# Optimization experiments

Measured on AMD Instinct MI355X. Metric: run time of the kernel, lower is better.

## Reference

```python
import jax, jax.numpy as jnp
import numpy as np

N = 100000        # nodes
E_RAND = 1600000  # random edges (avg degree 16)
D_IN = 64
D_OUT = 64


def setup_inputs() -> dict:
    key = jax.random.key(0)
    k1, k2, k3, k4, k5 = jax.random.split(key, 5)
    x = jax.random.normal(k1, (N, D_IN), dtype=jnp.float32)
    rows = jax.random.randint(k2, (E_RAND,), 0, N)
    cols = jax.random.randint(k3, (E_RAND,), 0, N)
    loops = jnp.arange(N)  # self loops appended at the end (matches remove+add_self_loops order)
    edge_index = jnp.stack([jnp.concatenate([rows, loops]),
                            jnp.concatenate([cols, loops])]).astype(jnp.int64)
    W = (jax.random.normal(k4, (D_IN, D_OUT), dtype=jnp.float32) / np.float32(np.sqrt(D_IN)))
    b = jax.random.normal(k5, (D_OUT,), dtype=jnp.float32) * 0.01
    return {"x": x, "edge_index": edge_index, "W": W, "b": b}


def reference(x, edge_index, W, b):
    row, col = edge_index[0], edge_index[1]
    # lin(x[row]) == (x @ W + b)[row]; transform once then gather (cheaper, same math)
    xl = x @ W + b                      # [N, D_OUT]
    x_i = xl[row]                       # [E, D_OUT] gather by destination
    x_j = xl[col]                       # [E, D_OUT] gather by source
    alpha = jnp.sum(x_i * x_j, axis=-1)  # [E] per-edge score
    alpha = jax.nn.leaky_relu(alpha, negative_slope=0.2)
    # segment-wise softmax over neighborhoods keyed by row
    m = jax.ops.segment_max(alpha, row, num_segments=N)
    m = jnp.where(jnp.isfinite(m), m, 0.0)   # isolated nodes -> -inf max, neutralize
    e = jnp.exp(alpha - m[row])
    s = jax.ops.segment_sum(e, row, num_segments=N)
    alpha = e / (s[row] + 1e-16)
    # dropout(p=0.6) skipped: reference runs in eval mode (deterministic)
    out = jax.ops.segment_sum(x_j * alpha[:, None], row, num_segments=N)  # [N, D_OUT]
    return out
```

## Files before the change

### kernel.cpp

```cpp
#include <hip/hip_runtime.h>
#include <hip/hip_bf16.h>


#define LEAKY_SLOPE 0.2f
#define BK_SHIFT 5
#define BK_NODES 32
#define CAPB 960
#define CH 8192
#define NBP 3136
#define MAXK 8

typedef __attribute__((ext_vector_type(8))) short short8;
typedef __attribute__((ext_vector_type(4))) float f32x4;

struct HiLo { short hi, lo; };

__device__ __forceinline__ HiLo split2(float f) {
    HiLo r;
    unsigned u = __float_as_uint(f);
    r.hi = (short)(u >> 16);
    float fh = __uint_as_float(u & 0xFFFF0000u);
    r.lo = (short)(__float_as_uint(f - fh) >> 16);
    return r;
}

__global__ __launch_bounds__(1024) void k_hist(const int* __restrict__ row,
                                               unsigned short* __restrict__ cntg,
                                               int E, int NB) {
    __shared__ int hc[NBP];
    int tid = threadIdx.x;
    for (int i = tid; i < NBP; i += 1024) hc[i] = 0;
    __syncthreads();
    int e0 = (int)blockIdx.x * CH;
    int e1 = min(E, e0 + CH);
    for (int e = e0 + tid; e < e1; e += 1024)
        atomicAdd(&hc[row[e] >> BK_SHIFT], 1);
    __syncthreads();
    unsigned short* orow = cntg + (size_t)blockIdx.x * NBP;
    for (int i = tid; i < NB; i += 1024) orow[i] = (unsigned short)hc[i];
}

__global__ __launch_bounds__(256) void k_tot(unsigned short* __restrict__ cntg,
                                             int* __restrict__ tot,
                                             int NB, int nch) {
    int wavegid = (((int)blockIdx.x * 256) + (int)threadIdx.x) >> 6;
    int lane = threadIdx.x & 63;
    int b = wavegid;
    if (b >= NB) return;

    int K = (nch + 63) >> 6;
    int v[MAXK];
    int s = 0;
    int c0 = lane * K;
#pragma unroll
    for (int k = 0; k < MAXK; ++k) {
        if (k < K) {
            int c = c0 + k;
            v[k] = (c < nch) ? (int)cntg[(size_t)c * NBP + b] : 0;
        }
    }
#pragma unroll
    for (int k = 0; k < MAXK; ++k) {
        if (k < K) { int t = v[k]; v[k] = s; s += t; }
    }
    int inc = s;
#pragma unroll
    for (int o = 1; o < 64; o <<= 1) {
        int t = __shfl_up(inc, o, 64);
        if (lane >= o) inc += t;
    }
    int exc = inc - s;
#pragma unroll
    for (int k = 0; k < MAXK; ++k) {
        if (k < K) {
            int c = c0 + k;
            if (c < nch)
                cntg[(size_t)c * NBP + b] = (unsigned short)(v[k] + exc);
        }
    }
    if (lane == 63) tot[b] = inc;
}

__global__ __launch_bounds__(1024) void k_base(const int* __restrict__ tot,
                                               int* __restrict__ base,
                                               int NB, int E) {
    __shared__ int segsum[16];
    int tid = threadIdx.x, lane = tid & 63, wid = tid >> 6;
    int segbeg = tid * 4;
    int loc[4];
    int s = 0;
#pragma unroll
    for (int k = 0; k < 4; ++k) {
        int i = segbeg + k;
        int t = (i < NB) ? tot[i] : 0;
        loc[k] = s; s += t;
    }
    int v = s;
#pragma unroll
    for (int o = 1; o < 64; o <<= 1) {
        int t = __shfl_up(v, o, 64);
        if (lane >= o) v += t;
    }
    if (lane == 63) segsum[wid] = v;
    __syncthreads();
    int woff = 0;
#pragma unroll
    for (int w = 0; w < 16; ++w) woff += (w < wid) ? segsum[w] : 0;
    int segoff = (v - s) + woff;
#pragma unroll
    for (int k = 0; k < 4; ++k) {
        int i = segbeg + k;
        if (i < NB) base[i] = loc[k] + segoff;
    }
    if (tid == 0) base[NB] = E;
}

union SLShMem {
    struct { short wt_hi[64 * 72]; short wt_lo[64 * 72]; } lin;
    struct { int pfx[NBP], pos[NBP]; } sc;
};

__global__ __launch_bounds__(1024) void k_scatlin(const float* __restrict__ x,
                                                  const float* __restrict__ W,
                                                  const float* __restrict__ b,
                                                  const int* __restrict__ row,
                                                  const int* __restrict__ col,
                                                  float* __restrict__ xl,
                                                  unsigned short* __restrict__ xlh,
                                                  const unsigned short* __restrict__ cntg,
                                                  const int* __restrict__ base,
                                                  unsigned* __restrict__ slab,
                                                  int N, int E, int NB,
                                                  int ntiles, int nsc, int nch) {
    __shared__ SLShMem sh;
    int tid = threadIdx.x;

    if ((int)blockIdx.x < nsc) {
        int cb = (int)blockIdx.x;
        int chunk = (nch % 8 == 0) ? (cb % 8) * (nch / 8) + cb / 8 : cb;

        const unsigned short* crow = cntg + (size_t)chunk * NBP;
        for (int i = tid; i < NB; i += 1024) {
            sh.sc.pfx[i] = base[i] + (int)crow[i];
            sh.sc.pos[i] = 0;
        }
        __syncthreads();

        int e0 = chunk * CH;
        int e1 = min(E, e0 + CH);
        for (int e = e0 + tid; e < e1; e += 1024) {
            int r = row[e], c = col[e];
            int bkt = r >> BK_SHIFT;
            int rank = atomicAdd(&sh.sc.pos[bkt], 1);
            slab[sh.sc.pfx[bkt] + rank] =
                ((unsigned)(r & (BK_NODES - 1)) << 17) | (unsigned)c;
        }
    } else {
        for (int i = tid; i < 4096; i += 1024) {
            int k = i >> 6, n = i & 63;
            HiLo h = split2(W[i]);
            sh.lin.wt_hi[n * 72 + k] = h.hi;
            sh.lin.wt_lo[n * 72 + k] = h.lo;
        }
        __syncthreads();

        int wave = tid >> 6, lane = tid & 63;
        int tile = ((int)blockIdx.x - nsc) * 16 + wave;
        if (tile >= ntiles) return;
        int node0 = tile * 16;
        int m = lane & 15;
        int quad = lane >> 4;

        f32x4 acc[4] = {{0.f, 0.f, 0.f, 0.f}, {0.f, 0.f, 0.f, 0.f},
                        {0.f, 0.f, 0.f, 0.f}, {0.f, 0.f, 0.f, 0.f}};

#pragma unroll
        for (int ks = 0; ks < 64; ks += 32) {
            const float* xr = x + (size_t)(node0 + m) * 64 + ks + quad * 8;
            float4 xa = *(const float4*)xr;
            float4 xb = *(const float4*)(xr + 4);
            short8 a_hi, a_lo;
            {
                HiLo h0 = split2(xa.x), h1 = split2(xa.y), h2 = split2(xa.z), h3 = split2(xa.w);
                HiLo h4 = split2(xb.x), h5 = split2(xb.y), h6 = split2(xb.z), h7 = split2(xb.w);
                a_hi[0] = h0.hi; a_lo[0] = h0.lo;  a_hi[1] = h1.hi; a_lo[1] = h1.lo;
                a_hi[2] = h2.hi; a_lo[2] = h2.lo;  a_hi[3] = h3.hi; a_lo[3] = h3.lo;
                a_hi[4] = h4.hi; a_lo[4] = h4.lo;  a_hi[5] = h5.hi; a_lo[5] = h5.lo;
                a_hi[6] = h6.hi; a_lo[6] = h6.lo;  a_hi[7] = h7.hi; a_lo[7] = h7.lo;
            }
#pragma unroll
            for (int g = 0; g < 4; ++g) {
                int n = g * 16 + m;
                int off = n * 72 + ks + quad * 8;
                short8 bh = *(const short8*)&sh.lin.wt_hi[off];
                short8 bl = *(const short8*)&sh.lin.wt_lo[off];
                acc[g] = __builtin_amdgcn_mfma_f32_16x16x32_bf16(a_hi, bh, acc[g], 0, 0, 0);
                acc[g] = __builtin_amdgcn_mfma_f32_16x16x32_bf16(a_lo, bh, acc[g], 0, 0, 0);
                acc[g] = __builtin_amdgcn_mfma_f32_16x16x32_bf16(a_hi, bl, acc[g], 0, 0, 0);
            }
        }

#pragma unroll
        for (int g = 0; g < 4; ++g) {
            float bias = b[g * 16 + m];
#pragma unroll
            for (int r = 0; r < 4; ++r) {
                int node = node0 + quad * 4 + r;
                if (node < N) {
                    float v = acc[g][r] + bias;
                    xl[(size_t)node * 64 + g * 16 + m] = v;
                    xlh[(size_t)node * 64 + g * 16 + m] =
                        (unsigned short)(__float_as_uint(v) >> 16);
                }
            }
        }
    }
}

template <int CTRL>
__device__ __forceinline__ float dpp_add(float x) {
    int y = __builtin_amdgcn_update_dpp(0, __float_as_int(x), CTRL, 0xF, 0xF, true);
    return x + __int_as_float(y);
}

__device__ __forceinline__ float red8(float d) {
    d = dpp_add<0xB1>(d);
    d = dpp_add<0x4E>(d);
    d = dpp_add<0x141>(d);
    return d;
}

__device__ __forceinline__ void bf8_to_f8(uint4 u, float4& a, float4& b) {
    a.x = __uint_as_float(u.x << 16);
    a.y = __uint_as_float(u.x & 0xFFFF0000u);
    a.z = __uint_as_float(u.y << 16);
    a.w = __uint_as_float(u.y & 0xFFFF0000u);
    b.x = __uint_as_float(u.z << 16);
    b.y = __uint_as_float(u.z & 0xFFFF0000u);
    b.z = __uint_as_float(u.w << 16);
    b.w = __uint_as_float(u.w & 0xFFFF0000u);
}

__device__ __forceinline__ float dot4(float4 a, float4 b) {
    return a.x * b.x + a.y * b.y + a.z * b.z + a.w * b.w;
}

__device__ __forceinline__ void edge_upd(int c, uint4 u, int node, float m,
                                         float4 xia, float4 xib,
                                         float& l, float4& A, float4& B) {
    float4 xa, xb;
    bf8_to_f8(u, xa, xb);
    float d = red8(dot4(xia, xa) + dot4(xib, xb));
    d = fmaxf(d, LEAKY_SLOPE * d);
    float p = __expf(d - m);
    p = (c != node) ? p : 0.0f;
    l += p;
    A.x += p * xa.x; A.y += p * xa.y; A.z += p * xa.z; A.w += p * xa.w;
    B.x += p * xb.x; B.y += p * xb.y; B.z += p * xb.z; B.w += p * xb.w;
}

__global__ __launch_bounds__(256) void k_agg(const float* __restrict__ xl,
                                             const unsigned short* __restrict__ xlh,
                                             const unsigned* __restrict__ slab,
                                             const int* __restrict__ base,
                                             float* __restrict__ out, int N) {
    __shared__ int raw[CAPB];
    __shared__ int colsh[CAPB];
    __shared__ int deg[BK_NODES], degp[BK_NODES], sc[BK_NODES];
    __shared__ int cur[BK_NODES], ord[BK_NODES];

    int bkt = blockIdx.x;
    int tid = threadIdx.x;

    int s0 = base[bkt];
    int cnt = base[bkt + 1] - s0;
    if (cnt > CAPB) cnt = CAPB;

    if (tid < BK_NODES) { deg[tid] = 0; cur[tid] = 0; }
    __syncthreads();

    const unsigned* sl = slab + s0;
    for (int i = tid; i < cnt; i += 256) {
        int e = (int)sl[i];
        raw[i] = e;
        atomicAdd(&deg[((unsigned)e) >> 17], 1);
    }
    __syncthreads();

    if (tid < BK_NODES) {
        int d = deg[tid];
        int dp = ((d + 5) / 6) * 6;
        degp[tid] = dp;
        int v = dp;
#pragma unroll
        for (int o = 1; o < 32; o <<= 1) {
            int t = __shfl_up(v, o, 32);
            if (tid >= o) v += t;
        }
        sc[tid] = v;
        int r = 0;
#pragma unroll
        for (int j = 0; j < BK_NODES; ++j) {
            int dj = deg[j];
            r += (dj > d) || (dj == d && j < tid);
        }
        ord[r] = tid;
    }
    __syncthreads();

    for (int i = tid; i < cnt; i += 256) {
        unsigned pk = (unsigned)raw[i];
        int rl = pk >> 17;
        int p = sc[rl] - degp[rl] + atomicAdd(&cur[rl], 1);
        colsh[p] = (int)(pk & 0x1FFFFu);
    }
    if (tid < BK_NODES) {
        int b0 = sc[tid] - degp[tid] + deg[tid];
        int b1 = sc[tid];
        int selfid = bkt * BK_NODES + tid;
        for (int i = b0; i < b1; ++i) colsh[i] = selfid;
    }
    __syncthreads();

    int grp = tid >> 3;
    int g = tid & 7;
    const uint4* xh4 = (const uint4*)xlh;
    int n0 = ord[grp];
    int node = bkt * BK_NODES + n0;
    if (node < N) {
        int e = sc[n0] - degp[n0];
        int end = sc[n0];
        float4 xia = ((const float4*)xl)[(size_t)node * 16 + 2 * g];
        float4 xib = ((const float4*)xl)[(size_t)node * 16 + 2 * g + 1];

        float mval = red8(dot4(xia, xia) + dot4(xib, xib));
        float l = 1.0f;
        float4 accA = xia;
        float4 accB = xib;

        int c0 = colsh[e],     c1 = colsh[e + 1], c2 = colsh[e + 2];
        int c3 = colsh[e + 3], c4 = colsh[e + 4], c5 = colsh[e + 5];
        uint4 u0 = xh4[(unsigned)(c0 * 8 + g)];
        uint4 u1 = xh4[(unsigned)(c1 * 8 + g)];
        uint4 u2 = xh4[(unsigned)(c2 * 8 + g)];
        uint4 u3 = xh4[(unsigned)(c3 * 8 + g)];
        uint4 u4 = xh4[(unsigned)(c4 * 8 + g)];
        uint4 u5 = xh4[(unsigned)(c5 * 8 + g)];

        for (; e + 12 <= end; e += 6) {
            edge_upd(c0, u0, node, mval, xia, xib, l, accA, accB);
            c0 = colsh[e + 6];  u0 = xh4[(unsigned)(c0 * 8 + g)];
            edge_upd(c1, u1, node, mval, xia, xib, l, accA, accB);
            c1 = colsh[e + 7];  u1 = xh4[(unsigned)(c1 * 8 + g)];
            edge_upd(c2, u2, node, mval, xia, xib, l, accA, accB);
            c2 = colsh[e + 8];  u2 = xh4[(unsigned)(c2 * 8 + g)];
            edge_upd(c3, u3, node, mval, xia, xib, l, accA, accB);
            c3 = colsh[e + 9];  u3 = xh4[(unsigned)(c3 * 8 + g)];
            edge_upd(c4, u4, node, mval, xia, xib, l, accA, accB);
            c4 = colsh[e + 10]; u4 = xh4[(unsigned)(c4 * 8 + g)];
            edge_upd(c5, u5, node, mval, xia, xib, l, accA, accB);
            c5 = colsh[e + 11]; u5 = xh4[(unsigned)(c5 * 8 + g)];
        }
        edge_upd(c0, u0, node, mval, xia, xib, l, accA, accB);
        edge_upd(c1, u1, node, mval, xia, xib, l, accA, accB);
        edge_upd(c2, u2, node, mval, xia, xib, l, accA, accB);
        edge_upd(c3, u3, node, mval, xia, xib, l, accA, accB);
        edge_upd(c4, u4, node, mval, xia, xib, l, accA, accB);
        edge_upd(c5, u5, node, mval, xia, xib, l, accA, accB);

        float inv = 1.0f / l;
        float4 oA = {accA.x * inv, accA.y * inv, accA.z * inv, accA.w * inv};
        float4 oB = {accB.x * inv, accB.y * inv, accB.z * inv, accB.w * inv};
        ((float4*)out)[(size_t)node * 16 + 2 * g] = oA;
        ((float4*)out)[(size_t)node * 16 + 2 * g + 1] = oB;
    }
}

extern "C" void kernel_launch(void* const* d_in, const int* in_sizes, int n_in,
                              void* d_out, int out_size, void* d_ws, size_t ws_size,
                              hipStream_t stream) {
    const float* x = (const float*)d_in[0];
    const int* ei = (const int*)d_in[1];
    const float* W = (const float*)d_in[2];
    const float* b = (const float*)d_in[3];

    const int N = in_sizes[0] / 64;
    const int E = in_sizes[1] / 2;
    const int NO = N * 64;
    const int NB = (N + BK_NODES - 1) >> BK_SHIFT;
    const int NCH = (E + CH - 1) / CH;
    const int* row = ei;
    const int* col = ei + E;

    float* out = (float*)d_out;

    float* ws = (float*)d_ws;
    float* xl           = ws;
    unsigned short* xlh = (unsigned short*)(xl + (size_t)NO);
    unsigned short* cntg= xlh + (size_t)NO;
    int* tot            = (int*)(cntg + (size_t)NCH * NBP);
    int* base           = tot + NB;
    unsigned* slab      = (unsigned*)(base + NB + 1);

    const int ntiles = (N + 15) / 16;
    const int lblocks = (ntiles + 15) / 16;

    k_hist<<<NCH, 1024, 0, stream>>>(row, cntg, E, NB);
    k_tot<<<(NB + 3) / 4, 256, 0, stream>>>(cntg, tot, NB, NCH);
    k_base<<<1, 1024, 0, stream>>>(tot, base, NB, E);
    k_scatlin<<<NCH + lblocks, 1024, 0, stream>>>(x, W, b, row, col, xl, xlh,
                                                  cntg, base, slab,
                                                  N, E, NB, ntiles, NCH, NCH);
    k_agg<<<NB, 256, 0, stream>>>(xl, xlh, slab, base, out, N);
}
```

Measured before the change: 165.0 us.

## Balance aggregation work by splitting edges into 6-edge slices across groups

Replaces the one-node-per-8-thread-group scheme, which needed a degree sort, with a flat list of 6-edge slices. Each slice is tagged with its owning node, and the 32 groups round-robin through all slices in the bucket. Partial softmax numerators and weighted sums go into shared memory with LDS atomics and are normalized at the end. This removes load imbalance from degree variance and the staging copy of raw edges, at the cost of shared-memory atomics per slice and a lower per-bucket edge cap.

```diff
diff --git a/kernel.cpp b/kernel.cpp
--- a/kernel.cpp
+++ b/kernel.cpp
@@ -245,7 +245,7 @@
     return a.x * b.x + a.y * b.y + a.z * b.z + a.w * b.w;
 }
 
-__device__ __forceinline__ void edge_upd(int c, uint4 u, int node, float m,
+__device__ __forceinline__ void edge_upd(int c, uint4 u, int selfid, float m,
                                          float4 xia, float4 xib,
                                          float& l, float4& A, float4& B) {
     float4 xa, xb;
@@ -253,7 +253,7 @@
     float d = red8(dot4(xia, xa) + dot4(xib, xb));
     d = fmaxf(d, LEAKY_SLOPE * d);
     float p = __expf(d - m);
-    p = (c != node) ? p : 0.0f;
+    p = (c != selfid) ? p : 0.0f;
     l += p;
     A.x += p * xa.x; A.y += p * xa.y; A.z += p * xa.z; A.w += p * xa.w;
     B.x += p * xb.x; B.y += p * xb.y; B.z += p * xb.z; B.w += p * xb.w;
@@ -264,27 +264,28 @@
                                              const unsigned* __restrict__ slab,
                                              const int* __restrict__ base,
                                              float* __restrict__ out, int N) {
-    __shared__ int raw[CAPB];
     __shared__ int colsh[CAPB];
-    __shared__ int deg[BK_NODES], degp[BK_NODES], sc[BK_NODES];
-    __shared__ int cur[BK_NODES], ord[BK_NODES];
+    __shared__ float accsh[BK_NODES * 64];
+    __shared__ float xish[BK_NODES * 64];
+    __shared__ float lsh[BK_NODES], msh[BK_NODES];
+    __shared__ int deg[BK_NODES], degp[BK_NODES], sc[BK_NODES], cur[BK_NODES];
+    __shared__ unsigned short slicenode[CAPB / 6];
 
     int bkt = blockIdx.x;
     int tid = threadIdx.x;
+    int grp = tid >> 3;
+    int g = tid & 7;
 
     int s0 = base[bkt];
     int cnt = base[bkt + 1] - s0;
-    if (cnt > CAPB) cnt = CAPB;
+    if (cnt > CAPB - 5 * BK_NODES) cnt = CAPB - 5 * BK_NODES;
 
     if (tid < BK_NODES) { deg[tid] = 0; cur[tid] = 0; }
     __syncthreads();
 
     const unsigned* sl = slab + s0;
-    for (int i = tid; i < cnt; i += 256) {
-        int e = (int)sl[i];
-        raw[i] = e;
-        atomicAdd(&deg[((unsigned)e) >> 17], 1);
-    }
+    for (int i = tid; i < cnt; i += 256)
+        atomicAdd(&deg[sl[i] >> 17], 1);
     __syncthreads();
 
     if (tid < BK_NODES) {
@@ -298,18 +299,11 @@
             if (tid >= o) v += t;
         }
         sc[tid] = v;
-        int r = 0;
-#pragma unroll
-        for (int j = 0; j < BK_NODES; ++j) {
-            int dj = deg[j];
-            r += (dj > d) || (dj == d && j < tid);
-        }
-        ord[r] = tid;
     }
     __syncthreads();
 
     for (int i = tid; i < cnt; i += 256) {
-        unsigned pk = (unsigned)raw[i];
+        unsigned pk = sl[i];
         int rl = pk >> 17;
         int p = sc[rl] - degp[rl] + atomicAdd(&cur[rl], 1);
         colsh[p] = (int)(pk & 0x1FFFFu);
@@ -319,27 +313,33 @@
         int b1 = sc[tid];
         int selfid = bkt * BK_NODES + tid;
         for (int i = b0; i < b1; ++i) colsh[i] = selfid;
-    }
-    __syncthreads();
-
-    int grp = tid >> 3;
-    int g = tid & 7;
+        int t0 = (sc[tid] - degp[tid]) / 6;
+        int nt = degp[tid] / 6;
+        for (int k = 0; k < nt; ++k) slicenode[t0 + k] = (unsigned short)tid;
+    }
+    {
+        int node = bkt * BK_NODES + grp;
+        float4 xia = {0.f, 0.f, 0.f, 0.f}, xib = {0.f, 0.f, 0.f, 0.f};
+        if (node < N) {
+            xia = ((const float4*)xl)[(size_t)node * 16 + 2 * g];
+            xib = ((const float4*)xl)[(size_t)node * 16 + 2 * g + 1];
+        }
+        *(float4*)&xish[grp * 64 + 8 * g]     = xia;
+        *(float4*)&xish[grp * 64 + 8 * g + 4] = xib;
+        *(float4*)&accsh[grp * 64 + 8 * g]     = xia;
+        *(float4*)&accsh[grp * 64 + 8 * g + 4] = xib;
+        float mv = red8(dot4(xia, xia) + dot4(xib, xib));
+        if (g == 0) { msh[grp] = mv; lsh[grp] = 1.0f; }
+    }
+    __syncthreads();
+
+    int T = sc[BK_NODES - 1] / 6;
     const uint4* xh4 = (const uint4*)xlh;
-    int n0 = ord[grp];
-    int node = bkt * BK_NODES + n0;
-    if (node < N) {
-        int e = sc[n0] - degp[n0];
-        int end = sc[n0];
-        float4 xia = ((const float4*)xl)[(size_t)node * 16 + 2 * g];
-        float4 xib = ((const float4*)xl)[(size_t)node * 16 + 2 * g + 1];
-
-        float mval = red8(dot4(xia, xia) + dot4(xib, xib));
-        float l = 1.0f;
-        float4 accA = xia;
-        float4 accB = xib;
-
-        int c0 = colsh[e],     c1 = colsh[e + 1], c2 = colsh[e + 2];
-        int c3 = colsh[e + 3], c4 = colsh[e + 4], c5 = colsh[e + 5];
+
+    if (grp < T) {
+        int t = grp;
+        int c0 = colsh[6 * t + 0], c1 = colsh[6 * t + 1], c2 = colsh[6 * t + 2];
+        int c3 = colsh[6 * t + 3], c4 = colsh[6 * t + 4], c5 = colsh[6 * t + 5];
         uint4 u0 = xh4[(unsigned)(c0 * 8 + g)];
         uint4 u1 = xh4[(unsigned)(c1 * 8 + g)];
         uint4 u2 = xh4[(unsigned)(c2 * 8 + g)];
@@ -347,32 +347,55 @@
         uint4 u4 = xh4[(unsigned)(c4 * 8 + g)];
         uint4 u5 = xh4[(unsigned)(c5 * 8 + g)];
 
-        for (; e + 12 <= end; e += 6) {
-            edge_upd(c0, u0, node, mval, xia, xib, l, accA, accB);
-            c0 = colsh[e + 6];  u0 = xh4[(unsigned)(c0 * 8 + g)];
-            edge_upd(c1, u1, node, mval, xia, xib, l, accA, accB);
-            c1 = colsh[e + 7];  u1 = xh4[(unsigned)(c1 * 8 + g)];
-            edge_upd(c2, u2, node, mval, xia, xib, l, accA, accB);
-            c2 = colsh[e + 8];  u2 = xh4[(unsigned)(c2 * 8 + g)];
-            edge_upd(c3, u3, node, mval, xia, xib, l, accA, accB);
-            c3 = colsh[e + 9];  u3 = xh4[(unsigned)(c3 * 8 + g)];
-            edge_upd(c4, u4, node, mval, xia, xib, l, accA, accB);
-            c4 = colsh[e + 10]; u4 = xh4[(unsigned)(c4 * 8 + g)];
-            edge_upd(c5, u5, node, mval, xia, xib, l, accA, accB);
-            c5 = colsh[e + 11]; u5 = xh4[(unsigned)(c5 * 8 + g)];
-        }
-        edge_upd(c0, u0, node, mval, xia, xib, l, accA, accB);
-        edge_upd(c1, u1, node, mval, xia, xib, l, accA, accB);
-        edge_upd(c2, u2, node, mval, xia, xib, l, accA, accB);
-        edge_upd(c3, u3, node, mval, xia, xib, l, accA, accB);
-        edge_upd(c4, u4, node, mval, xia, xib, l, accA, accB);
-        edge_upd(c5, u5, node, mval, xia, xib, l, accA, accB);
-
-        float inv = 1.0f / l;
-        float4 oA = {accA.x * inv, accA.y * inv, accA.z * inv, accA.w * inv};
-        float4 oB = {accB.x * inv, accB.y * inv, accB.z * inv, accB.w * inv};
-        ((float4*)out)[(size_t)node * 16 + 2 * g] = oA;
-        ((float4*)out)[(size_t)node * 16 + 2 * g + 1] = oB;
+        while (t < T) {
+            int n = slicenode[t];
+            float mv = msh[n];
+            int selfid = bkt * BK_NODES + n;
+            float4 xia = *(const float4*)&xish[n * 64 + 8 * g];
+            float4 xib = *(const float4*)&xish[n * 64 + 8 * g + 4];
+            float lp = 0.f;
+            float4 pA = {0.f, 0.f, 0.f, 0.f}, pB = {0.f, 0.f, 0.f, 0.f};
+
+            int tn = t + 32;
+            int tl = (tn < T) ? tn : t;
+            int eb = 6 * tl;
+
+            edge_upd(c0, u0, selfid, mv, xia, xib, lp, pA, pB);
+            c0 = colsh[eb + 0]; u0 = xh4[(unsigned)(c0 * 8 + g)];
+            edge_upd(c1, u1, selfid, mv, xia, xib, lp, pA, pB);
+            c1 = colsh[eb + 1]; u1 = xh4[(unsigned)(c1 * 8 + g)];
+            edge_upd(c2, u2, selfid, mv, xia, xib, lp, pA, pB);
+            c2 = colsh[eb + 2]; u2 = xh4[(unsigned)(c2 * 8 + g)];
+            edge_upd(c3, u3, selfid, mv, xia, xib, lp, pA, pB);
+            c3 = colsh[eb + 3]; u3 = xh4[(unsigned)(c3 * 8 + g)];
+            edge_upd(c4, u4, selfid, mv, xia, xib, lp, pA, pB);
+            c4 = colsh[eb + 4]; u4 = xh4[(unsigned)(c4 * 8 + g)];
+            edge_upd(c5, u5, selfid, mv, xia, xib, lp, pA, pB);
+            c5 = colsh[eb + 5]; u5 = xh4[(unsigned)(c5 * 8 + g)];
+
+            float* an = &accsh[n * 64 + 8 * g];
+            atomicAdd(&an[0], pA.x); atomicAdd(&an[1], pA.y);
+            atomicAdd(&an[2], pA.z); atomicAdd(&an[3], pA.w);
+            atomicAdd(&an[4], pB.x); atomicAdd(&an[5], pB.y);
+            atomicAdd(&an[6], pB.z); atomicAdd(&an[7], pB.w);
+            if (g == 0) atomicAdd(&lsh[n], lp);
+
+            t = tn;
+        }
+    }
+    __syncthreads();
+
+    {
+        int node = bkt * BK_NODES + grp;
+        if (node < N) {
+            float inv = 1.0f / lsh[grp];
+            float4 oA = *(float4*)&accsh[grp * 64 + 8 * g];
+            float4 oB = *(float4*)&accsh[grp * 64 + 8 * g + 4];
+            oA.x *= inv; oA.y *= inv; oA.z *= inv; oA.w *= inv;
+            oB.x *= inv; oB.y *= inv; oB.z *= inv; oB.w *= inv;
+            ((float4*)out)[(size_t)node * 16 + 2 * g] = oA;
+            ((float4*)out)[(size_t)node * 16 + 2 * g + 1] = oB;
+        }
     }
 }
 
```

Result: slower. 260.8 us (+58.1%).
